# Performance work log

Hardware: AMD Instinct MI355X
Metric: run time of the kernel (lower is better)

## Reference

```python
import jax, jax.numpy as jnp
import numpy as np

GAMMA = 0.99
ENTROPY_COEF = 0.01
GAE_LAMBDA = 0.95
VALUE_LOSS_COEF = 0.5

T = 65536          # agent rollout length
O, S, A = 8, 1048576, 6  # opponents, steps, actions


def setup_inputs() -> dict:
    key = jax.random.key(0)
    ks = jax.random.split(key, 9)
    return {
        "agent_rewards": jax.random.normal(ks[0], (T,), jnp.float32),
        "agent_log_probs": jax.random.normal(ks[1], (T,), jnp.float32),
        "agent_values": jax.random.normal(ks[2], (T + 1,), jnp.float32),
        "agent_entropies": jax.random.uniform(ks[3], (T,), jnp.float32),
        "opponent_log_probs": jax.random.normal(ks[4], (O, S, A), jnp.float32),
        "opponent_actions_ground_truths": jax.random.randint(ks[5], (O, S), 0, A),
        "opponent_values": jax.random.normal(ks[6], (O, S), jnp.float32),
        "opponent_rewards": jax.random.normal(ks[7], (O, S - 1), jnp.float32),
        "opponent_coefs": jax.random.uniform(ks[8], (O,), jnp.float32),
    }


def _agent_loss(rewards, values, log_probs, entropies):
    # Sequential GAE / discounted-return recurrence, scanned from last step to first.
    def step(carry, xs):
        R, gae, pl, vl = carry
        r, v, v_next, lp, ent = xs
        R = GAMMA * R + r
        adv = R - v
        vl = vl + 0.5 * adv * adv
        delta = r + GAMMA * v_next - v
        gae = gae * GAMMA * GAE_LAMBDA + delta
        pl = pl - lp * jax.lax.stop_gradient(gae) - ENTROPY_COEF * ent
        return (R, gae, pl, vl), None

    init = (values[-1], jnp.float32(0.0), jnp.float32(0.0), jnp.float32(0.0))
    xs = (rewards, values[:-1], values[1:], log_probs, entropies)
    (_, _, pl, vl), _ = jax.lax.scan(step, init, xs, reverse=True)
    return pl + VALUE_LOSS_COEF * vl


def _opponent_loss(log_probs, actions, values, rewards, coefs):
    # cross_entropy in torch applies log_softmax to its input, even though the arg
    # is (mis)named log_probs -> ce = mean(logsumexp(logits) - logits[target])
    logZ = jax.nn.logsumexp(log_probs, axis=-1)                      # (O, S)
    tgt = jnp.take_along_axis(log_probs, actions[..., None], axis=-1)[..., 0]
    ce = jnp.mean(logZ - tgt, axis=-1)                               # (O,)
    policy_loss = coefs * ce

    v0 = values[:, :-1]                                              # (O, S-1)
    v_next = values[:, 1:]                                           # roll(-1) then truncate
    pred = rewards + GAMMA * v_next
    d = v0 - pred
    ad = jnp.abs(d)
    sl1 = jnp.mean(jnp.where(ad < 1.0, 0.5 * d * d, ad - 0.5), axis=-1)
    value_loss = coefs * sl1
    return jnp.sum(policy_loss + value_loss)


def reference(agent_rewards, agent_log_probs, agent_values, agent_entropies,
              opponent_log_probs, opponent_actions_ground_truths,
              opponent_values, opponent_rewards, opponent_coefs):
    agent_loss = _agent_loss(agent_rewards, agent_values, agent_log_probs, agent_entropies)
    opp_loss = _opponent_loss(opponent_log_probs, opponent_actions_ground_truths,
                              opponent_values, opponent_rewards, opponent_coefs)
    return jnp.sum(agent_loss + opp_loss)
```

## Files before the change

### kernel.cpp

```cpp
#include <hip/hip_runtime.h>
#include <cstddef>

constexpr float GAMMA = 0.99f;
constexpr float GLAM  = 0.99f * 0.95f;
constexpr float ENT_C = 0.01f;

constexpr int T = 65536;
constexpr int O = 8;
constexpr int S = 1048576;
constexpr int A = 6;
constexpr int BLK = 256;

constexpr int BPO        = 512;
constexpr int OPP_BLOCKS = O * BPO;
constexpr int ROWS_PER_B = S / BPO;
constexpr int STAGE_ROWS = 512;
constexpr int NSTAGE     = ROWS_PER_B / STAGE_ROWS;
constexpr int CHUNK      = T / BLK;


__device__ __forceinline__ float row_ce(float l0, float l1, float l2,
                                        float l3, float l4, float l5, int a)
{
    float m  = fmaxf(fmaxf(fmaxf(l0, l1), fmaxf(l2, l3)), fmaxf(l4, l5));
    float se = __expf(l0 - m) + __expf(l1 - m) + __expf(l2 - m) +
               __expf(l3 - m) + __expf(l4 - m) + __expf(l5 - m);
    float tgt = (a == 0) ? l0 : (a == 1) ? l1 : (a == 2) ? l2 :
                (a == 3) ? l3 : (a == 4) ? l4 : l5;
    return (m + __logf(se)) - tgt;
}

__global__ __launch_bounds__(BLK)
void fused_kernel(const float* __restrict__ arew,
                  const float* __restrict__ alp,
                  const float* __restrict__ aval,
                  const float* __restrict__ aent,
                  const float* __restrict__ olp,
                  const int*   __restrict__ oact,
                  const float* __restrict__ oval,
                  const float* __restrict__ orew,
                  float* __restrict__ ws)
{
    const int tid = threadIdx.x;
    __shared__ float s1[BLK], s2[BLK];

    if (blockIdx.x == 0) {
        const int base = tid * CHUNK;

        float cR = 0.f, cG = 0.f;
        float nextv = aval[base + CHUNK];
        #pragma unroll 4
        for (int k4 = CHUNK - 4; k4 >= 0; k4 -= 4) {
            float4 r4 = *reinterpret_cast<const float4*>(&arew[base + k4]);
            float4 v4 = *reinterpret_cast<const float4*>(&aval[base + k4]);
            cR = GAMMA * cR + r4.w;  cG = GLAM * cG + (r4.w + GAMMA * nextv - v4.w);
            cR = GAMMA * cR + r4.z;  cG = GLAM * cG + (r4.z + GAMMA * v4.w  - v4.z);
            cR = GAMMA * cR + r4.y;  cG = GLAM * cG + (r4.y + GAMMA * v4.z  - v4.y);
            cR = GAMMA * cR + r4.x;  cG = GLAM * cG + (r4.x + GAMMA * v4.y  - v4.x);
            nextv = v4.x;
        }
        s1[tid] = cR; s2[tid] = cG;
        __syncthreads();

        if (tid == 0) {
            double aRd = 1.0, aGd = 1.0;
            for (int i = 0; i < CHUNK; ++i) { aRd *= 0.99; aGd *= 0.99 * 0.95; }
            const float aR = (float)aRd, aG = (float)aGd;
            float Rin = aval[T];
            float Gin = 0.f;
            for (int i = BLK - 1; i >= 0; --i) {
                float cr = s1[i], cg = s2[i];
                s1[i] = Rin; s2[i] = Gin;
                Rin = aR * Rin + cr;
                Gin = aG * Gin + cg;
            }
        }
        __syncthreads();
        float R = s1[tid], g = s2[tid];
        __syncthreads();

        float pl = 0.f, vl = 0.f;
        nextv = aval[base + CHUNK];
        #pragma unroll 4
        for (int k4 = CHUNK - 4; k4 >= 0; k4 -= 4) {
            float4 r4 = *reinterpret_cast<const float4*>(&arew[base + k4]);
            float4 v4 = *reinterpret_cast<const float4*>(&aval[base + k4]);
            float4 l4 = *reinterpret_cast<const float4*>(&alp [base + k4]);
            float4 e4 = *reinterpret_cast<const float4*>(&aent[base + k4]);

            R = GAMMA * R + r4.w; { float adv = R - v4.w; vl += 0.5f * adv * adv; }
            g = GLAM * g + (r4.w + GAMMA * nextv - v4.w); pl += -l4.w * g - ENT_C * e4.w;
            R = GAMMA * R + r4.z; { float adv = R - v4.z; vl += 0.5f * adv * adv; }
            g = GLAM * g + (r4.z + GAMMA * v4.w  - v4.z); pl += -l4.z * g - ENT_C * e4.z;
            R = GAMMA * R + r4.y; { float adv = R - v4.y; vl += 0.5f * adv * adv; }
            g = GLAM * g + (r4.y + GAMMA * v4.z  - v4.y); pl += -l4.y * g - ENT_C * e4.y;
            R = GAMMA * R + r4.x; { float adv = R - v4.x; vl += 0.5f * adv * adv; }
            g = GLAM * g + (r4.x + GAMMA * v4.y  - v4.x); pl += -l4.x * g - ENT_C * e4.x;
            nextv = v4.x;
        }
        s1[tid] = pl; s2[tid] = vl;
        __syncthreads();
        for (int stp = BLK / 2; stp > 0; stp >>= 1) {
            if (tid < stp) { s1[tid] += s1[tid + stp]; s2[tid] += s2[tid + stp]; }
            __syncthreads();
        }
        if (tid == 0) ws[2 * OPP_BLOCKS] = s1[0] + 0.5f * s2[0];
        return;
    }

    __shared__ float lds[STAGE_ROWS * A];

    const int bid  = blockIdx.x - 1;
    const int o    = bid / BPO;
    const int seg  = bid % BPO;
    const int row0 = seg * ROWS_PER_B;
    const size_t obase = (size_t)o * S;
    const size_t rbase = (size_t)o * (S - 1);

    float4 pa, pb, pc; int2 pact; float2 pv; float pv2, pr0, pr1;

    auto issue = [&](int s) {
        const int srow = row0 + s * STAGE_ROWS;
        const float4* lp4 = reinterpret_cast<const float4*>(olp + (obase + srow) * (size_t)A);
        pa = lp4[tid];
        pb = lp4[tid + BLK];
        pc = lp4[tid + 2 * BLK];
        const int r = srow + 2 * tid;
        const size_t gr = obase + r;
        pact = *reinterpret_cast<const int2*>(&oact[gr]);
        pv   = *reinterpret_cast<const float2*>(&oval[gr]);
        pv2  = (r + 2 <= S - 1) ? oval[gr + 2] : 0.f;
        pr0  = orew[rbase + r];
        pr1  = (r + 1 < S - 1) ? orew[rbase + r + 1] : 0.f;
    };

    float ce_acc = 0.f, sl_acc = 0.f;
    issue(0);

    #pragma unroll
    for (int s = 0; s < NSTAGE; ++s) {
        __syncthreads();
        reinterpret_cast<float4*>(lds)[tid]           = pa;
        reinterpret_cast<float4*>(lds)[tid + BLK]     = pb;
        reinterpret_cast<float4*>(lds)[tid + 2 * BLK] = pc;
        const int2  act = pact;
        const float2 v  = pv;
        const float v2 = pv2, rw0 = pr0, rw1 = pr1;
        const int r = row0 + s * STAGE_ROWS + 2 * tid;
        if (s + 1 < NSTAGE) issue(s + 1);
        __syncthreads();

        const float* lrow = &lds[12 * tid];
        float4 q0 = *reinterpret_cast<const float4*>(lrow);
        float4 q1 = *reinterpret_cast<const float4*>(lrow + 4);
        float4 q2 = *reinterpret_cast<const float4*>(lrow + 8);

        ce_acc += row_ce(q0.x, q0.y, q0.z, q0.w, q1.x, q1.y, act.x);
        ce_acc += row_ce(q1.z, q1.w, q2.x, q2.y, q2.z, q2.w, act.y);

        {
            float d  = v.x - (rw0 + GAMMA * v.y);
            float ad = fabsf(d);
            sl_acc += (ad < 1.f) ? 0.5f * d * d : ad - 0.5f;
        }
        if (r + 1 < S - 1) {
            float d  = v.y - (rw1 + GAMMA * v2);
            float ad = fabsf(d);
            sl_acc += (ad < 1.f) ? 0.5f * d * d : ad - 0.5f;
        }
    }

    s1[tid] = ce_acc; s2[tid] = sl_acc;
    __syncthreads();
    for (int stp = BLK / 2; stp > 0; stp >>= 1) {
        if (tid < stp) { s1[tid] += s1[tid + stp]; s2[tid] += s2[tid + stp]; }
        __syncthreads();
    }
    if (tid == 0) {
        ws[bid]              = s1[0];
        ws[OPP_BLOCKS + bid] = s2[0];
    }
}

__global__ __launch_bounds__(BLK)
void finalize_kernel(const float* __restrict__ ws,
                     const float* __restrict__ coefs,
                     float* __restrict__ out)
{
    const int tid = threadIdx.x;
    __shared__ float r1[BLK], r2[BLK];
    float tot = 0.f;
    for (int o = 0; o < O; ++o) {
        const float* cw = ws + o * (BPO);
        const float* sw = ws + OPP_BLOCKS + o * BPO;
        r1[tid] = cw[tid] + cw[tid + BLK];
        r2[tid] = sw[tid] + sw[tid + BLK];
        __syncthreads();
        for (int stp = BLK / 2; stp > 0; stp >>= 1) {
            if (tid < stp) { r1[tid] += r1[tid + stp]; r2[tid] += r2[tid + stp]; }
            __syncthreads();
        }
        if (tid == 0)
            tot += coefs[o] * (r1[0] / (float)S + r2[0] / (float)(S - 1));
        __syncthreads();
    }
    if (tid == 0) out[0] = tot + ws[2 * OPP_BLOCKS];
}

extern "C" void kernel_launch(void* const* d_in, const int* in_sizes, int n_in,
                              void* d_out, int out_size, void* d_ws, size_t ws_size,
                              hipStream_t stream)
{
    const float* arew  = (const float*)d_in[0];
    const float* alp   = (const float*)d_in[1];
    const float* aval  = (const float*)d_in[2];
    const float* aent  = (const float*)d_in[3];
    const float* olp   = (const float*)d_in[4];
    const int*   oact  = (const int*)  d_in[5];
    const float* oval  = (const float*)d_in[6];
    const float* orew  = (const float*)d_in[7];
    const float* ocoef = (const float*)d_in[8];
    float* ws = (float*)d_ws;

    fused_kernel<<<1 + OPP_BLOCKS, BLK, 0, stream>>>(arew, alp, aval, aent,
                                                     olp, oact, oval, orew, ws);
    finalize_kernel<<<1, BLK, 0, stream>>>(ws, ocoef, (float*)d_out);
}
```

Measured before the change: 100.8 us.

## Replace LDS-staged opponent loop with direct per-thread vector nontemporal loads

The opponent path no longer stages log-prob rows through shared memory over multiple stages with barriers. Each thread now loads four contiguous rows in each of two halves straight into registers, using 16-byte nontemporal loads for logits, actions, values and rewards. This removes the LDS round trip and the per-stage syncthreads, and issues every load up front to increase memory-level parallelism. In exchange it uses more registers per thread, and the per-thread accesses are strided by 96 bytes, which may coalesce less well than the earlier fully contiguous float4 stage loads.

Result: slower. 118.9 us (+17.9%).

```diff
diff --git a/kernel.cpp b/kernel.cpp
--- a/kernel.cpp
+++ b/kernel.cpp
@@ -8,15 +8,18 @@
 constexpr int T = 65536;
 constexpr int O = 8;
 constexpr int S = 1048576;
-constexpr int A = 6;
 constexpr int BLK = 256;
 
 constexpr int BPO        = 512;
 constexpr int OPP_BLOCKS = O * BPO;
 constexpr int ROWS_PER_B = S / BPO;
-constexpr int STAGE_ROWS = 512;
-constexpr int NSTAGE     = ROWS_PER_B / STAGE_ROWS;
 constexpr int CHUNK      = T / BLK;
+
+typedef float f4 __attribute__((ext_vector_type(4)));
+typedef int   i4 __attribute__((ext_vector_type(4)));
+
+template <typename Tp>
+__device__ __forceinline__ Tp ntload(const Tp* p) { return __builtin_nontemporal_load(p); }
 
 
 __device__ __forceinline__ float row_ce(float l0, float l1, float l2,
@@ -28,6 +31,13 @@
     float tgt = (a == 0) ? l0 : (a == 1) ? l1 : (a == 2) ? l2 :
                 (a == 3) ? l3 : (a == 4) ? l4 : l5;
     return (m + __logf(se)) - tgt;
+}
+
+__device__ __forceinline__ float sl1(float v0, float v1, float rw)
+{
+    float d  = v0 - (rw + GAMMA * v1);
+    float ad = fabsf(d);
+    return (ad < 1.f) ? 0.5f * d * d : ad - 0.5f;
 }
 
 __global__ __launch_bounds__(BLK)
@@ -108,67 +118,57 @@
         return;
     }
 
-    __shared__ float lds[STAGE_ROWS * A];
-
     const int bid  = blockIdx.x - 1;
-    const int o    = bid / BPO;
-    const int seg  = bid % BPO;
+    const int o    = bid >> 9;
+    const int seg  = bid & (BPO - 1);
     const int row0 = seg * ROWS_PER_B;
     const size_t obase = (size_t)o * S;
     const size_t rbase = (size_t)o * (S - 1);
 
-    float4 pa, pb, pc; int2 pact; float2 pv; float pv2, pr0, pr1;
-
-    auto issue = [&](int s) {
-        const int srow = row0 + s * STAGE_ROWS;
-        const float4* lp4 = reinterpret_cast<const float4*>(olp + (obase + srow) * (size_t)A);
-        pa = lp4[tid];
-        pb = lp4[tid + BLK];
-        pc = lp4[tid + 2 * BLK];
-        const int r = srow + 2 * tid;
-        const size_t gr = obase + r;
-        pact = *reinterpret_cast<const int2*>(&oact[gr]);
-        pv   = *reinterpret_cast<const float2*>(&oval[gr]);
-        pv2  = (r + 2 <= S - 1) ? oval[gr + 2] : 0.f;
-        pr0  = orew[rbase + r];
-        pr1  = (r + 1 < S - 1) ? orew[rbase + r + 1] : 0.f;
-    };
+    const int r1 = row0 + 4 * tid;
+    const int r2 = row0 + (ROWS_PER_B / 2) + 4 * tid;
+
+    const f4* Lp1 = reinterpret_cast<const f4*>(olp + (obase + r1) * 6);
+    const f4* Lp2 = reinterpret_cast<const f4*>(olp + (obase + r2) * 6);
+    f4 a0 = ntload(Lp1 + 0), a1 = ntload(Lp1 + 1), a2 = ntload(Lp1 + 2);
+    f4 a3 = ntload(Lp1 + 3), a4 = ntload(Lp1 + 4), a5 = ntload(Lp1 + 5);
+    f4 b0 = ntload(Lp2 + 0), b1 = ntload(Lp2 + 1), b2 = ntload(Lp2 + 2);
+    f4 b3 = ntload(Lp2 + 3), b4 = ntload(Lp2 + 4), b5 = ntload(Lp2 + 5);
+
+    i4 A1 = ntload(reinterpret_cast<const i4*>(oact + obase + r1));
+    i4 A2 = ntload(reinterpret_cast<const i4*>(oact + obase + r2));
+    f4 V1 = ntload(reinterpret_cast<const f4*>(oval + obase + r1));
+    f4 V2 = ntload(reinterpret_cast<const f4*>(oval + obase + r2));
+    float V1e = oval[obase + r1 + 4];
+    float V2e = (r2 + 4 <= S - 1) ? oval[obase + r2 + 4] : 0.f;
+    float w10 = ntload(orew + rbase + r1);
+    float w11 = ntload(orew + rbase + r1 + 1);
+    float w12 = ntload(orew + rbase + r1 + 2);
+    float w13 = ntload(orew + rbase + r1 + 3);
+    float w20 = ntload(orew + rbase + r2);
+    float w21 = ntload(orew + rbase + r2 + 1);
+    float w22 = ntload(orew + rbase + r2 + 2);
+    float w23 = (r2 + 3 < S - 1) ? orew[rbase + r2 + 3] : 0.f;
 
     float ce_acc = 0.f, sl_acc = 0.f;
-    issue(0);
-
-    #pragma unroll
-    for (int s = 0; s < NSTAGE; ++s) {
-        __syncthreads();
-        reinterpret_cast<float4*>(lds)[tid]           = pa;
-        reinterpret_cast<float4*>(lds)[tid + BLK]     = pb;
-        reinterpret_cast<float4*>(lds)[tid + 2 * BLK] = pc;
-        const int2  act = pact;
-        const float2 v  = pv;
-        const float v2 = pv2, rw0 = pr0, rw1 = pr1;
-        const int r = row0 + s * STAGE_ROWS + 2 * tid;
-        if (s + 1 < NSTAGE) issue(s + 1);
-        __syncthreads();
-
-        const float* lrow = &lds[12 * tid];
-        float4 q0 = *reinterpret_cast<const float4*>(lrow);
-        float4 q1 = *reinterpret_cast<const float4*>(lrow + 4);
-        float4 q2 = *reinterpret_cast<const float4*>(lrow + 8);
-
-        ce_acc += row_ce(q0.x, q0.y, q0.z, q0.w, q1.x, q1.y, act.x);
-        ce_acc += row_ce(q1.z, q1.w, q2.x, q2.y, q2.z, q2.w, act.y);
-
-        {
-            float d  = v.x - (rw0 + GAMMA * v.y);
-            float ad = fabsf(d);
-            sl_acc += (ad < 1.f) ? 0.5f * d * d : ad - 0.5f;
-        }
-        if (r + 1 < S - 1) {
-            float d  = v.y - (rw1 + GAMMA * v2);
-            float ad = fabsf(d);
-            sl_acc += (ad < 1.f) ? 0.5f * d * d : ad - 0.5f;
-        }
-    }
+
+    ce_acc += row_ce(a0[0], a0[1], a0[2], a0[3], a1[0], a1[1], A1[0]);
+    ce_acc += row_ce(a1[2], a1[3], a2[0], a2[1], a2[2], a2[3], A1[1]);
+    ce_acc += row_ce(a3[0], a3[1], a3[2], a3[3], a4[0], a4[1], A1[2]);
+    ce_acc += row_ce(a4[2], a4[3], a5[0], a5[1], a5[2], a5[3], A1[3]);
+    ce_acc += row_ce(b0[0], b0[1], b0[2], b0[3], b1[0], b1[1], A2[0]);
+    ce_acc += row_ce(b1[2], b1[3], b2[0], b2[1], b2[2], b2[3], A2[1]);
+    ce_acc += row_ce(b3[0], b3[1], b3[2], b3[3], b4[0], b4[1], A2[2]);
+    ce_acc += row_ce(b4[2], b4[3], b5[0], b5[1], b5[2], b5[3], A2[3]);
+
+    sl_acc += sl1(V1[0], V1[1], w10);
+    sl_acc += sl1(V1[1], V1[2], w11);
+    sl_acc += sl1(V1[2], V1[3], w12);
+    sl_acc += sl1(V1[3], V1e,   w13);
+    sl_acc += sl1(V2[0], V2[1], w20);
+    sl_acc += sl1(V2[1], V2[2], w21);
+    sl_acc += sl1(V2[2], V2[3], w22);
+    if (r2 + 3 < S - 1) sl_acc += sl1(V2[3], V2e, w23);
 
     s1[tid] = ce_acc; s2[tid] = sl_acc;
     __syncthreads();
@@ -191,7 +191,7 @@
     __shared__ float r1[BLK], r2[BLK];
     float tot = 0.f;
     for (int o = 0; o < O; ++o) {
-        const float* cw = ws + o * (BPO);
+        const float* cw = ws + o * BPO;
         const float* sw = ws + OPP_BLOCKS + o * BPO;
         r1[tid] = cw[tid] + cw[tid + BLK];
         r2[tid] = sw[tid] + sw[tid + BLK];
```
